# Kernel optimization log

Measured on AMD Instinct MI355X. Metric: run time of the kernel, lower is better.

## Reference

```python
import jax, jax.numpy as jnp
import numpy as np

N_HEAD = 16
QMIN, QMAX = 0.0, 255.0  # 8-bit asymmetric


def fake_quantize(x, scale, zp):
    # LearnableFakeQuantize (asymmetric, 8-bit) with straight-through round.
    q = x / scale + zp
    q = q + jax.lax.stop_gradient(jnp.round(q) - q)  # STE round
    q = jnp.clip(q, QMIN, QMAX)
    return (q - zp) * scale


def setup_inputs() -> dict:
    key = jax.random.key(0)
    ks = jax.random.split(key, 4)
    B, T, C = 2, 2048, 1024
    return {
        "hidden_states": jax.random.normal(ks[0], (B, T, C), jnp.float32),
        "W_attn": jax.random.normal(ks[1], (C, 3 * C), jnp.float32) * (1.0 / np.sqrt(C)),
        "b_attn": jnp.zeros((3 * C,), jnp.float32),
        "W_proj": jax.random.normal(ks[2], (C, C), jnp.float32) * (1.0 / np.sqrt(C)),
        "b_proj": jnp.zeros((C,), jnp.float32),
        "kv_scale": jnp.full((1,), 0.05, jnp.float32),
        "kv_zp": jnp.full((1,), 128.0, jnp.float32),
    }


def reference(hidden_states, W_attn, b_attn, W_proj, b_proj, kv_scale, kv_zp):
    B, T, C = hidden_states.shape
    H = N_HEAD
    D = C // H
    qkv = hidden_states @ W_attn + b_attn            # [B,T,3C]
    q, k, v = jnp.split(qkv, 3, axis=2)
    # [B,T,C] -> [B,H,T,D]
    q = q.reshape(B, T, H, D).transpose(0, 2, 1, 3)
    k = k.reshape(B, T, H, D).transpose(0, 2, 1, 3)
    v = v.reshape(B, T, H, D).transpose(0, 2, 1, 3)
    k = fake_quantize(k, kv_scale, kv_zp)
    v = fake_quantize(v, kv_scale, kv_zp)
    scores = jnp.einsum("bhqd,bhkd->bhqk", q, k) / jnp.sqrt(jnp.asarray(D, q.dtype))
    causal = jnp.tril(jnp.ones((T, T), bool))        # bias[:T,:T]
    scores = jnp.where(causal, scores, jnp.asarray(-jnp.inf, scores.dtype))
    attn = jax.nn.softmax(scores, axis=-1)
    out = jnp.einsum("bhqk,bhkd->bhqd", attn, v)     # [B,H,T,D]
    out = out.transpose(0, 2, 1, 3).reshape(B, T, C)
    return out @ W_proj + b_proj
```

## Files before the change

### kernel.cpp

```cpp
#include <hip/hip_runtime.h>
#include <math.h>

#define TB 2048
#define CC 1024
#define NH 16
#define HD 64

typedef __bf16 bf16x8 __attribute__((ext_vector_type(8)));
typedef __bf16 bf16x4 __attribute__((ext_vector_type(4)));
typedef float  f32x4  __attribute__((ext_vector_type(4)));

__device__ inline float exp2fast(float x) { return __builtin_amdgcn_exp2f(x); }

__device__ __forceinline__ void gl_lds16(const __bf16* g, __bf16* l) {
    __builtin_amdgcn_global_load_lds(
        (const __attribute__((address_space(1))) void*)g,
        (__attribute__((address_space(3))) void*)l, 16, 0, 0);
}

__global__ __launch_bounds__(256)
void prep_kernel(const float* __restrict__ hidden, __bf16* __restrict__ hb,
                 const float* __restrict__ Wa, __bf16* __restrict__ wat,
                 const float* __restrict__ Wp, __bf16* __restrict__ wpt)
{
    __shared__ __bf16 L[64][68];
    const int tid = threadIdx.x;
    const int bid = blockIdx.x;
    if (bid < 4096) {
        int i = (bid * 256 + tid) * 4;
        f32x4 v = *(const f32x4*)&hidden[i];
        bf16x4 o;
        o.x = (__bf16)v.x; o.y = (__bf16)v.y; o.z = (__bf16)v.z; o.w = (__bf16)v.w;
        *(bf16x4*)&hb[i] = o;
        return;
    }
    const float* src; __bf16* dst; int N, n0, k0;
    if (bid < 4096 + 768) {
        int t = bid - 4096;
        src = Wa; dst = wat; N = 3072;
        n0 = (t % 48) * 64; k0 = (t / 48) * 64;
    } else {
        int t = bid - 4864;
        src = Wp; dst = wpt; N = 1024;
        n0 = (t % 16) * 64; k0 = (t / 16) * 64;
    }
    #pragma unroll
    for (int i = 0; i < 4; i++) {
        int id = tid + i * 256;
        int r = id >> 4, c = (id & 15) * 4;
        f32x4 v = *(const f32x4*)&src[(size_t)(k0 + r) * N + n0 + c];
        bf16x4 o;
        o.x = (__bf16)v.x; o.y = (__bf16)v.y; o.z = (__bf16)v.z; o.w = (__bf16)v.w;
        *(bf16x4*)&L[r][c] = o;
    }
    __syncthreads();
    #pragma unroll
    for (int i = 0; i < 4; i++) {
        int id = tid + i * 256;
        int nr = id >> 4, kc = (id & 15) * 4;
        bf16x4 o;
        o.x = L[kc + 0][nr]; o.y = L[kc + 1][nr];
        o.z = L[kc + 2][nr]; o.w = L[kc + 3][nr];
        *(bf16x4*)&dst[(size_t)(n0 + nr) * 1024 + k0 + kc] = o;
    }
}

template<int BN, int MODE>
__global__ __launch_bounds__(256)
void gemm_bt(const __bf16* __restrict__ A, const __bf16* __restrict__ Bt,
             const float* __restrict__ bias,
             __bf16* __restrict__ o0, __bf16* __restrict__ o1,
             __bf16* __restrict__ o2, float* __restrict__ of,
             int M, int N, int K,
             const float* __restrict__ scp, const float* __restrict__ zpp)
{
    constexpr int NT = BN / 32;
    __shared__ __bf16 Asm[128][64];
    __shared__ __bf16 Bsm[BN][64];

    const int tid  = threadIdx.x;
    const int m0   = blockIdx.y * 128;
    const int n0   = blockIdx.x * BN;
    const int w    = tid >> 6, lane = tid & 63;
    const int wm   = (w & 1) * 64, wn = (w >> 1) * (BN / 2);
    const int r16  = lane & 15, quad = lane >> 4;
    const int srow = lane >> 3;
    const int scol = ((lane & 7) ^ srow) * 8;
    const int rsw  = r16 & 7;

    f32x4 acc[NT][4];
    #pragma unroll
    for (int i = 0; i < NT; i++)
        #pragma unroll
        for (int j = 0; j < 4; j++) acc[i][j] = 0.f;

    for (int k0 = 0; k0 < K; k0 += 64) {
        #pragma unroll
        for (int p = 0; p < 4; p++)
            gl_lds16(&A[(size_t)(m0 + w * 32 + p * 8 + srow) * K + k0 + scol],
                     &Asm[w * 32 + p * 8][0]);
        #pragma unroll
        for (int p = 0; p < BN / 32; p++)
            gl_lds16(&Bt[(size_t)(n0 + w * (BN / 4) + p * 8 + srow) * K + k0 + scol],
                     &Bsm[w * (BN / 4) + p * 8][0]);
        __syncthreads();

        #pragma unroll
        for (int ks = 0; ks < 2; ks++) {
            const int col = ((ks * 4 + quad) ^ rsw) * 8;
            bf16x8 af[4], bfr[NT];
            #pragma unroll
            for (int mt = 0; mt < 4; mt++)
                af[mt] = *(const bf16x8*)&Asm[wm + mt * 16 + r16][col];
            #pragma unroll
            for (int nt = 0; nt < NT; nt++)
                bfr[nt] = *(const bf16x8*)&Bsm[wn + nt * 16 + r16][col];
            #pragma unroll
            for (int nt = 0; nt < NT; nt++)
                #pragma unroll
                for (int mt = 0; mt < 4; mt++)
                    acc[nt][mt] = __builtin_amdgcn_mfma_f32_16x16x32_bf16(
                        bfr[nt], af[mt], acc[nt][mt], 0, 0, 0);
        }
        __syncthreads();
    }

    const float sc = scp[0];
    const float zp = zpp[0];

    #pragma unroll
    for (int nt = 0; nt < NT; nt++) {
        #pragma unroll
        for (int mt = 0; mt < 4; mt++) {
            int gm = m0 + wm + mt * 16 + r16;
            int gn = n0 + wn + nt * 16 + quad * 4;
            f32x4 val = acc[nt][mt] + *(const f32x4*)&bias[gn];
            if (MODE == 1) {
                *(f32x4*)&of[(size_t)gm * N + gn] = val;
            } else {
                int part = gn >> 10;
                int idx  = gn & 1023;
                int h = idx >> 6, d = idx & 63;
                int b = gm >> 11, t = gm & 2047;
                size_t off = (((size_t)(b * NH + h)) * TB + t) * HD + d;
                bf16x4 st;
                if (part == 0) {
                    #pragma unroll
                    for (int r = 0; r < 4; r++)
                        st[r] = (__bf16)(val[r] * 0.18033688f);
                    *(bf16x4*)&o0[off] = st;
                } else {
                    #pragma unroll
                    for (int r = 0; r < 4; r++) {
                        float qv = val[r] / sc + zp;
                        qv = rintf(qv);
                        qv = fminf(fmaxf(qv, 0.f), 255.f);
                        st[r] = (__bf16)((qv - zp) * sc);
                    }
                    if (part == 1) *(bf16x4*)&o1[off] = st;
                    else           *(bf16x4*)&o2[off] = st;
                }
            }
        }
    }
}

__global__ __launch_bounds__(256, 4)
void attn_mfma(const __bf16* __restrict__ Q, const __bf16* __restrict__ Kg,
               const __bf16* __restrict__ Vg, __bf16* __restrict__ O)
{
    __shared__ alignas(16) __bf16 Ksm[64][72];
    __shared__ alignas(16) __bf16 Vsm[64][72];

    const int tid  = threadIdx.x;
    const int qt   = 31 - (blockIdx.x >> 5);
    const int bh   = blockIdx.x & 31;
    const int q0   = qt * 64;
    const int w    = tid >> 6, lane = tid & 63;
    const int l15  = lane & 15, quad = lane >> 4;
    const int b    = bh >> 4, h = bh & 15;

    const int krow = tid >> 3;
    const int kseg = (tid & 7) * 8;
    const int vkey = tid & 63;
    const int vc   = tid >> 6;

    const __bf16* Kbh = Kg + (size_t)bh * TB * HD;
    const __bf16* Vbh = Vg + (size_t)bh * TB * HD;

    const __bf16* Qrow = Q + ((size_t)bh * TB + q0 + w * 16 + l15) * HD;
    bf16x8 qf0 = *(const bf16x8*)&Qrow[quad * 8];
    bf16x8 qf1 = *(const bf16x8*)&Qrow[32 + quad * 8];

    const int rbase = (l15 >> 2) * 8 + (l15 & 3);

    bf16x8 af_l;
    {
        __bf16 v = (l15 == 0) ? (__bf16)1.0f : (__bf16)0.0f;
        #pragma unroll
        for (int j = 0; j < 8; j++) af_l[j] = v;
    }

    f32x4 acc_o[4], acc_l;
    #pragma unroll
    for (int nt = 0; nt < 4; nt++) acc_o[nt] = 0.f;
    acc_l = 0.f;
    float mrun = -3.0e38f;

    bf16x8 kpre0 = *(const bf16x8*)&Kbh[(size_t)krow * HD + kseg];
    bf16x8 kpre1 = *(const bf16x8*)&Kbh[(size_t)(32 + krow) * HD + kseg];
    bf16x8 vpre0 = *(const bf16x8*)&Vbh[(size_t)vkey * HD + vc * 8];
    bf16x8 vpre1 = *(const bf16x8*)&Vbh[(size_t)vkey * HD + (4 + vc) * 8];

    for (int kt = 0; kt <= qt; kt++) {
        __syncthreads();
        *(bf16x8*)&Ksm[krow][kseg]      = kpre0;
        *(bf16x8*)&Ksm[32 + krow][kseg] = kpre1;
        #pragma unroll
        for (int j = 0; j < 8; j++) {
            Vsm[vc * 8 + j][vkey]      = vpre0[j];
            Vsm[32 + vc * 8 + j][vkey] = vpre1[j];
        }
        __syncthreads();

        if (kt < qt) {
            const __bf16* Kn = Kbh + (size_t)(kt + 1) * 64 * HD;
            const __bf16* Vn = Vbh + (size_t)(kt + 1) * 64 * HD;
            kpre0 = *(const bf16x8*)&Kn[(size_t)krow * HD + kseg];
            kpre1 = *(const bf16x8*)&Kn[(size_t)(32 + krow) * HD + kseg];
            vpre0 = *(const bf16x8*)&Vn[(size_t)vkey * HD + vc * 8];
            vpre1 = *(const bf16x8*)&Vn[(size_t)vkey * HD + (4 + vc) * 8];
        }

        const bool diag = (kt == qt);

        f32x4 s[4];
        #pragma unroll
        for (int nt = 0; nt < 4; nt++) s[nt] = 0.f;
        #pragma unroll
        for (int nt = 0; nt < 4; nt++) {
            if (diag && (nt & 1) && w < 2) continue;
            int row = rbase + (nt & 1) * 32 + ((nt >> 1) << 2);
            bf16x8 kf0 = *(const bf16x8*)&Ksm[row][quad * 8];
            bf16x8 kf1 = *(const bf16x8*)&Ksm[row][32 + quad * 8];
            s[nt] = __builtin_amdgcn_mfma_f32_16x16x32_bf16(kf0, qf0, s[nt], 0, 0, 0);
            s[nt] = __builtin_amdgcn_mfma_f32_16x16x32_bf16(kf1, qf1, s[nt], 0, 0, 0);
        }

        if (diag) {
            #pragma unroll
            for (int nt = 0; nt < 4; nt++) {
                int koff = (nt & 1) * 32 + ((nt >> 1) << 2) + quad * 8;
                #pragma unroll
                for (int r = 0; r < 4; r++)
                    if (koff + r > w * 16 + l15) s[nt][r] = -3.0e38f;
            }
        }

        float mx = s[0][0];
        #pragma unroll
        for (int nt = 0; nt < 4; nt++)
            #pragma unroll
            for (int r = 0; r < 4; r++) mx = fmaxf(mx, s[nt][r]);
        mx = fmaxf(mx, __shfl_xor(mx, 16));
        mx = fmaxf(mx, __shfl_xor(mx, 32));

        float mnew  = fmaxf(mrun, mx);
        float alpha = exp2fast(mrun - mnew);
        mrun = mnew;
        #pragma unroll
        for (int nt = 0; nt < 4; nt++)
            #pragma unroll
            for (int r = 0; r < 4; r++) acc_o[nt][r] *= alpha;
        acc_l[0] *= alpha;

        float p[4][4];
        #pragma unroll
        for (int nt = 0; nt < 4; nt++)
            #pragma unroll
            for (int r = 0; r < 4; r++) p[nt][r] = exp2fast(s[nt][r] - mnew);

        bf16x8 pf0, pf1;
        #pragma unroll
        for (int j = 0; j < 4; j++) {
            pf0[j]     = (__bf16)p[0][j];
            pf0[4 + j] = (__bf16)p[2][j];
            pf1[j]     = (__bf16)p[1][j];
            pf1[4 + j] = (__bf16)p[3][j];
        }

        acc_l = __builtin_amdgcn_mfma_f32_16x16x32_bf16(af_l, pf0, acc_l, 0, 0, 0);
        acc_l = __builtin_amdgcn_mfma_f32_16x16x32_bf16(af_l, pf1, acc_l, 0, 0, 0);

        #pragma unroll
        for (int nt = 0; nt < 4; nt++) {
            bf16x8 vf0 = *(const bf16x8*)&Vsm[nt * 16 + l15][quad * 8];
            bf16x8 vf1 = *(const bf16x8*)&Vsm[nt * 16 + l15][32 + quad * 8];
            acc_o[nt] = __builtin_amdgcn_mfma_f32_16x16x32_bf16(vf0, pf0, acc_o[nt], 0, 0, 0);
            acc_o[nt] = __builtin_amdgcn_mfma_f32_16x16x32_bf16(vf1, pf1, acc_o[nt], 0, 0, 0);
        }
    }

    float lall = __shfl(acc_l[0], l15);
    float inv  = 1.f / lall;
    size_t trow = (size_t)(b * TB) + q0 + w * 16 + l15;
    #pragma unroll
    for (int nt = 0; nt < 4; nt++) {
        bf16x4 st;
        #pragma unroll
        for (int r = 0; r < 4; r++) st[r] = (__bf16)(acc_o[nt][r] * inv);
        *(bf16x4*)&O[trow * CC + h * HD + nt * 16 + quad * 4] = st;
    }
}

extern "C" void kernel_launch(void* const* d_in, const int* in_sizes, int n_in,
                              void* d_out, int out_size, void* d_ws, size_t ws_size,
                              hipStream_t stream) {
    (void)in_sizes; (void)n_in; (void)out_size; (void)ws_size;
    const float* hidden   = (const float*)d_in[0];
    const float* W_attn   = (const float*)d_in[1];
    const float* b_attn   = (const float*)d_in[2];
    const float* W_proj   = (const float*)d_in[3];
    const float* b_proj   = (const float*)d_in[4];
    const float* kv_scale = (const float*)d_in[5];
    const float* kv_zp    = (const float*)d_in[6];
    float* out = (float*)d_out;

    __bf16* hb  = (__bf16*)d_ws;
    __bf16* wat = hb  + (size_t)4096 * 1024;
    __bf16* wpt = wat + (size_t)3072 * 1024;
    __bf16* qws = wpt + (size_t)1024 * 1024;
    __bf16* kws = qws + (size_t)2 * NH * TB * HD;
    __bf16* vws = kws + (size_t)2 * NH * TB * HD;
    __bf16* ows = vws + (size_t)2 * NH * TB * HD;

    prep_kernel<<<5120, 256, 0, stream>>>(hidden, hb, W_attn, wat, W_proj, wpt);

    gemm_bt<128, 0><<<dim3(24, 32), 256, 0, stream>>>(
        hb, wat, b_attn, qws, kws, vws, nullptr, 4096, 3072, 1024, kv_scale, kv_zp);

    attn_mfma<<<dim3(32 * 32), 256, 0, stream>>>(qws, kws, vws, ows);

    gemm_bt<64, 1><<<dim3(16, 32), 256, 0, stream>>>(
        ows, wpt, b_proj, nullptr, nullptr, nullptr, out, 4096, 1024, 1024,
        kv_scale, kv_zp);
}
```

Baseline: 182.3 us.

## Use 128-row query tiles in attention and store V transposed from QKV GEMM

The attention kernel now processes 128 query rows per block, with each wave handling two 16-row chunks, so every K/V tile loaded into shared memory serves twice as many queries. Blocks are ordered to interleave heavy and light causal tiles. The QKV GEMM epilogue writes V in a transposed [d][t] layout, which lets attention stage V with vector shared-memory stores instead of scalar transposing writes. K rows are permuted on store so fragment reads become contiguous. In exchange, the transposed V epilogue uses scattered 2-byte global stores, register use per thread grows, and only half as many blocks are launched.

```diff
diff --git a/kernel.cpp b/kernel.cpp
--- a/kernel.cpp
+++ b/kernel.cpp
@@ -142,9 +142,9 @@
                 int idx  = gn & 1023;
                 int h = idx >> 6, d = idx & 63;
                 int b = gm >> 11, t = gm & 2047;
-                size_t off = (((size_t)(b * NH + h)) * TB + t) * HD + d;
                 bf16x4 st;
                 if (part == 0) {
+                    size_t off = (((size_t)(b * NH + h)) * TB + t) * HD + d;
                     #pragma unroll
                     for (int r = 0; r < 4; r++)
                         st[r] = (__bf16)(val[r] * 0.18033688f);
@@ -157,42 +157,53 @@
                         qv = fminf(fmaxf(qv, 0.f), 255.f);
                         st[r] = (__bf16)((qv - zp) * sc);
                     }
-                    if (part == 1) *(bf16x4*)&o1[off] = st;
-                    else           *(bf16x4*)&o2[off] = st;
+                    if (part == 1) {
+                        size_t off = (((size_t)(b * NH + h)) * TB + t) * HD + d;
+                        *(bf16x4*)&o1[off] = st;
+                    } else {
+                        size_t offv = (((size_t)(b * NH + h)) * HD + d) * TB + t;
+                        #pragma unroll
+                        for (int r = 0; r < 4; r++)
+                            o2[offv + (size_t)r * TB] = st[r];
+                    }
                 }
             }
         }
     }
 }
 
-__global__ __launch_bounds__(256, 4)
+__global__ __launch_bounds__(256)
 void attn_mfma(const __bf16* __restrict__ Q, const __bf16* __restrict__ Kg,
-               const __bf16* __restrict__ Vg, __bf16* __restrict__ O)
+               const __bf16* __restrict__ Vt, __bf16* __restrict__ O)
 {
     __shared__ alignas(16) __bf16 Ksm[64][72];
     __shared__ alignas(16) __bf16 Vsm[64][72];
 
-    const int tid  = threadIdx.x;
-    const int qt   = 31 - (blockIdx.x >> 5);
-    const int bh   = blockIdx.x & 31;
-    const int q0   = qt * 64;
-    const int w    = tid >> 6, lane = tid & 63;
-    const int l15  = lane & 15, quad = lane >> 4;
-    const int b    = bh >> 4, h = bh & 15;
-
-    const int krow = tid >> 3;
-    const int kseg = (tid & 7) * 8;
-    const int vkey = tid & 63;
-    const int vc   = tid >> 6;
+    const int tid = threadIdx.x;
+    const int bid = blockIdx.x;
+    const int qb  = (bid < 256) ? 15 - (bid >> 5) : ((bid - 256) >> 5);
+    const int bh  = bid & 31;
+    const int q0  = qb * 128;
+    const int ktmax = 2 * qb + 1;
+    const int w   = tid >> 6, lane = tid & 63;
+    const int l15 = lane & 15, quad = lane >> 4;
+    const int b   = bh >> 4, h = bh & 15;
+
+    const int srow = tid >> 3;
+    const int sseg = (tid & 7) * 8;
+    const int p0 = ((srow >> 2) & 1) * 32 + ((srow >> 3) & 3) * 4 + (srow & 3);
+    const int p1 = p0 + 16;
 
     const __bf16* Kbh = Kg + (size_t)bh * TB * HD;
-    const __bf16* Vbh = Vg + (size_t)bh * TB * HD;
-
-    const __bf16* Qrow = Q + ((size_t)bh * TB + q0 + w * 16 + l15) * HD;
-    bf16x8 qf0 = *(const bf16x8*)&Qrow[quad * 8];
-    bf16x8 qf1 = *(const bf16x8*)&Qrow[32 + quad * 8];
-
-    const int rbase = (l15 >> 2) * 8 + (l15 & 3);
+    const __bf16* Vbh = Vt + (size_t)bh * HD * TB;
+
+    bf16x8 qf[2][2];
+    #pragma unroll
+    for (int c = 0; c < 2; c++) {
+        const __bf16* Qrow = Q + ((size_t)bh * TB + q0 + w * 32 + c * 16 + l15) * HD;
+        qf[c][0] = *(const bf16x8*)&Qrow[quad * 8];
+        qf[c][1] = *(const bf16x8*)&Qrow[32 + quad * 8];
+    }
 
     bf16x8 af_l;
     {
@@ -201,115 +212,141 @@
         for (int j = 0; j < 8; j++) af_l[j] = v;
     }
 
-    f32x4 acc_o[4], acc_l;
-    #pragma unroll
-    for (int nt = 0; nt < 4; nt++) acc_o[nt] = 0.f;
-    acc_l = 0.f;
-    float mrun = -3.0e38f;
-
-    bf16x8 kpre0 = *(const bf16x8*)&Kbh[(size_t)krow * HD + kseg];
-    bf16x8 kpre1 = *(const bf16x8*)&Kbh[(size_t)(32 + krow) * HD + kseg];
-    bf16x8 vpre0 = *(const bf16x8*)&Vbh[(size_t)vkey * HD + vc * 8];
-    bf16x8 vpre1 = *(const bf16x8*)&Vbh[(size_t)vkey * HD + (4 + vc) * 8];
-
-    for (int kt = 0; kt <= qt; kt++) {
+    f32x4 acc_o[2][4], acc_l[2];
+    #pragma unroll
+    for (int c = 0; c < 2; c++) {
+        #pragma unroll
+        for (int nt = 0; nt < 4; nt++) acc_o[c][nt] = 0.f;
+        acc_l[c] = 0.f;
+    }
+    float mrun[2] = {-3.0e38f, -3.0e38f};
+
+    bf16x8 kpre0 = *(const bf16x8*)&Kbh[(size_t)srow * HD + sseg];
+    bf16x8 kpre1 = *(const bf16x8*)&Kbh[(size_t)(32 + srow) * HD + sseg];
+    bf16x8 vpre0 = *(const bf16x8*)&Vbh[(size_t)srow * TB + sseg];
+    bf16x8 vpre1 = *(const bf16x8*)&Vbh[(size_t)(32 + srow) * TB + sseg];
+
+    for (int kt = 0; kt <= ktmax; kt++) {
         __syncthreads();
-        *(bf16x8*)&Ksm[krow][kseg]      = kpre0;
-        *(bf16x8*)&Ksm[32 + krow][kseg] = kpre1;
-        #pragma unroll
-        for (int j = 0; j < 8; j++) {
-            Vsm[vc * 8 + j][vkey]      = vpre0[j];
-            Vsm[32 + vc * 8 + j][vkey] = vpre1[j];
-        }
+        *(bf16x8*)&Ksm[p0][sseg]        = kpre0;
+        *(bf16x8*)&Ksm[p1][sseg]        = kpre1;
+        *(bf16x8*)&Vsm[srow][sseg]      = vpre0;
+        *(bf16x8*)&Vsm[32 + srow][sseg] = vpre1;
         __syncthreads();
 
-        if (kt < qt) {
+        if (kt < ktmax) {
             const __bf16* Kn = Kbh + (size_t)(kt + 1) * 64 * HD;
-            const __bf16* Vn = Vbh + (size_t)(kt + 1) * 64 * HD;
-            kpre0 = *(const bf16x8*)&Kn[(size_t)krow * HD + kseg];
-            kpre1 = *(const bf16x8*)&Kn[(size_t)(32 + krow) * HD + kseg];
-            vpre0 = *(const bf16x8*)&Vn[(size_t)vkey * HD + vc * 8];
-            vpre1 = *(const bf16x8*)&Vn[(size_t)vkey * HD + (4 + vc) * 8];
-        }
-
-        const bool diag = (kt == qt);
-
-        f32x4 s[4];
-        #pragma unroll
-        for (int nt = 0; nt < 4; nt++) s[nt] = 0.f;
+            kpre0 = *(const bf16x8*)&Kn[(size_t)srow * HD + sseg];
+            kpre1 = *(const bf16x8*)&Kn[(size_t)(32 + srow) * HD + sseg];
+            const int cb = (kt + 1) * 64;
+            vpre0 = *(const bf16x8*)&Vbh[(size_t)srow * TB + cb + sseg];
+            vpre1 = *(const bf16x8*)&Vbh[(size_t)(32 + srow) * TB + cb + sseg];
+        }
+
+        const int kbase = kt * 64;
+        const int qmax0 = q0 + w * 32 + 15;
+        const int qmax1 = qmax0 + 16;
+        const bool act0 = (kbase <= qmax0);
+        const bool act1 = (kbase <= qmax1);
+
+        f32x4 s[2][4];
+        #pragma unroll
+        for (int c = 0; c < 2; c++)
+            #pragma unroll
+            for (int nt = 0; nt < 4; nt++) s[c][nt] = 0.f;
         #pragma unroll
         for (int nt = 0; nt < 4; nt++) {
-            if (diag && (nt & 1) && w < 2) continue;
-            int row = rbase + (nt & 1) * 32 + ((nt >> 1) << 2);
-            bf16x8 kf0 = *(const bf16x8*)&Ksm[row][quad * 8];
-            bf16x8 kf1 = *(const bf16x8*)&Ksm[row][32 + quad * 8];
-            s[nt] = __builtin_amdgcn_mfma_f32_16x16x32_bf16(kf0, qf0, s[nt], 0, 0, 0);
-            s[nt] = __builtin_amdgcn_mfma_f32_16x16x32_bf16(kf1, qf1, s[nt], 0, 0, 0);
-        }
-
-        if (diag) {
-            #pragma unroll
-            for (int nt = 0; nt < 4; nt++) {
-                int koff = (nt & 1) * 32 + ((nt >> 1) << 2) + quad * 8;
-                #pragma unroll
-                for (int r = 0; r < 4; r++)
-                    if (koff + r > w * 16 + l15) s[nt][r] = -3.0e38f;
-            }
-        }
-
-        float mx = s[0][0];
-        #pragma unroll
-        for (int nt = 0; nt < 4; nt++)
-            #pragma unroll
-            for (int r = 0; r < 4; r++) mx = fmaxf(mx, s[nt][r]);
-        mx = fmaxf(mx, __shfl_xor(mx, 16));
-        mx = fmaxf(mx, __shfl_xor(mx, 32));
-
-        float mnew  = fmaxf(mrun, mx);
-        float alpha = exp2fast(mrun - mnew);
-        mrun = mnew;
-        #pragma unroll
-        for (int nt = 0; nt < 4; nt++)
-            #pragma unroll
-            for (int r = 0; r < 4; r++) acc_o[nt][r] *= alpha;
-        acc_l[0] *= alpha;
-
-        float p[4][4];
-        #pragma unroll
-        for (int nt = 0; nt < 4; nt++)
-            #pragma unroll
-            for (int r = 0; r < 4; r++) p[nt][r] = exp2fast(s[nt][r] - mnew);
-
-        bf16x8 pf0, pf1;
-        #pragma unroll
-        for (int j = 0; j < 4; j++) {
-            pf0[j]     = (__bf16)p[0][j];
-            pf0[4 + j] = (__bf16)p[2][j];
-            pf1[j]     = (__bf16)p[1][j];
-            pf1[4 + j] = (__bf16)p[3][j];
-        }
-
-        acc_l = __builtin_amdgcn_mfma_f32_16x16x32_bf16(af_l, pf0, acc_l, 0, 0, 0);
-        acc_l = __builtin_amdgcn_mfma_f32_16x16x32_bf16(af_l, pf1, acc_l, 0, 0, 0);
+            const int kmin = kbase + (nt & 1) * 32 + ((nt >> 1) << 2);
+            if (kmin > qmax1) continue;
+            bf16x8 kf0 = *(const bf16x8*)&Ksm[nt * 16 + l15][quad * 8];
+            bf16x8 kf1 = *(const bf16x8*)&Ksm[nt * 16 + l15][32 + quad * 8];
+            if (act0 && kmin <= qmax0) {
+                s[0][nt] = __builtin_amdgcn_mfma_f32_16x16x32_bf16(kf0, qf[0][0], s[0][nt], 0, 0, 0);
+                s[0][nt] = __builtin_amdgcn_mfma_f32_16x16x32_bf16(kf1, qf[0][1], s[0][nt], 0, 0, 0);
+            }
+            if (act1) {
+                s[1][nt] = __builtin_amdgcn_mfma_f32_16x16x32_bf16(kf0, qf[1][0], s[1][nt], 0, 0, 0);
+                s[1][nt] = __builtin_amdgcn_mfma_f32_16x16x32_bf16(kf1, qf[1][1], s[1][nt], 0, 0, 0);
+            }
+        }
+
+        bf16x8 pf[2][2];
+        #pragma unroll
+        for (int c = 0; c < 2; c++) {
+            const bool act = c ? act1 : act0;
+            if (!act) continue;
+            const int qlo = q0 + w * 32 + c * 16;
+            if (kbase + 63 > qlo) {
+                const int qg = qlo + l15;
+                #pragma unroll
+                for (int nt = 0; nt < 4; nt++) {
+                    const int koff = kbase + (nt & 1) * 32 + ((nt >> 1) << 2) + quad * 8;
+                    #pragma unroll
+                    for (int r = 0; r < 4; r++)
+                        if (koff + r > qg) s[c][nt][r] = -3.0e38f;
+                }
+            }
+            float mx = s[c][0][0];
+            #pragma unroll
+            for (int nt = 0; nt < 4; nt++)
+                #pragma unroll
+                for (int r = 0; r < 4; r++) mx = fmaxf(mx, s[c][nt][r]);
+            mx = fmaxf(mx, __shfl_xor(mx, 16));
+            mx = fmaxf(mx, __shfl_xor(mx, 32));
+
+            float mnew  = fmaxf(mrun[c], mx);
+            float alpha = exp2fast(mrun[c] - mnew);
+            mrun[c] = mnew;
+            #pragma unroll
+            for (int nt = 0; nt < 4; nt++)
+                #pragma unroll
+                for (int r = 0; r < 4; r++) acc_o[c][nt][r] *= alpha;
+            acc_l[c][0] *= alpha;
+
+            float p[4][4];
+            #pragma unroll
+            for (int nt = 0; nt < 4; nt++)
+                #pragma unroll
+                for (int r = 0; r < 4; r++) p[nt][r] = exp2fast(s[c][nt][r] - mnew);
+
+            #pragma unroll
+            for (int j = 0; j < 4; j++) {
+                pf[c][0][j]     = (__bf16)p[0][j];
+                pf[c][0][4 + j] = (__bf16)p[2][j];
+                pf[c][1][j]     = (__bf16)p[1][j];
+                pf[c][1][4 + j] = (__bf16)p[3][j];
+            }
+            acc_l[c] = __builtin_amdgcn_mfma_f32_16x16x32_bf16(af_l, pf[c][0], acc_l[c], 0, 0, 0);
+            acc_l[c] = __builtin_amdgcn_mfma_f32_16x16x32_bf16(af_l, pf[c][1], acc_l[c], 0, 0, 0);
+        }
 
         #pragma unroll
         for (int nt = 0; nt < 4; nt++) {
             bf16x8 vf0 = *(const bf16x8*)&Vsm[nt * 16 + l15][quad * 8];
             bf16x8 vf1 = *(const bf16x8*)&Vsm[nt * 16 + l15][32 + quad * 8];
-            acc_o[nt] = __builtin_amdgcn_mfma_f32_16x16x32_bf16(vf0, pf0, acc_o[nt], 0, 0, 0);
-            acc_o[nt] = __builtin_amdgcn_mfma_f32_16x16x32_bf16(vf1, pf1, acc_o[nt], 0, 0, 0);
-        }
-    }
-
-    float lall = __shfl(acc_l[0], l15);
-    float inv  = 1.f / lall;
-    size_t trow = (size_t)(b * TB) + q0 + w * 16 + l15;
-    #pragma unroll
-    for (int nt = 0; nt < 4; nt++) {
-        bf16x4 st;
-        #pragma unroll
-        for (int r = 0; r < 4; r++) st[r] = (__bf16)(acc_o[nt][r] * inv);
-        *(bf16x4*)&O[trow * CC + h * HD + nt * 16 + quad * 4] = st;
+            if (act0) {
+                acc_o[0][nt] = __builtin_amdgcn_mfma_f32_16x16x32_bf16(vf0, pf[0][0], acc_o[0][nt], 0, 0, 0);
+                acc_o[0][nt] = __builtin_amdgcn_mfma_f32_16x16x32_bf16(vf1, pf[0][1], acc_o[0][nt], 0, 0, 0);
+            }
+            if (act1) {
+                acc_o[1][nt] = __builtin_amdgcn_mfma_f32_16x16x32_bf16(vf0, pf[1][0], acc_o[1][nt], 0, 0, 0);
+                acc_o[1][nt] = __builtin_amdgcn_mfma_f32_16x16x32_bf16(vf1, pf[1][1], acc_o[1][nt], 0, 0, 0);
+            }
+        }
+    }
+
+    #pragma unroll
+    for (int c = 0; c < 2; c++) {
+        float lall = __shfl(acc_l[c][0], l15);
+        float inv  = 1.f / lall;
+        size_t trow = (size_t)(b * TB) + q0 + w * 32 + c * 16 + l15;
+        #pragma unroll
+        for (int nt = 0; nt < 4; nt++) {
+            bf16x4 st;
+            #pragma unroll
+            for (int r = 0; r < 4; r++) st[r] = (__bf16)(acc_o[c][nt][r] * inv);
+            *(bf16x4*)&O[trow * CC + h * HD + nt * 16 + quad * 4] = st;
+        }
     }
 }
 
@@ -339,7 +376,7 @@
     gemm_bt<128, 0><<<dim3(24, 32), 256, 0, stream>>>(
         hb, wat, b_attn, qws, kws, vws, nullptr, 4096, 3072, 1024, kv_scale, kv_zp);
 
-    attn_mfma<<<dim3(32 * 32), 256, 0, stream>>>(qws, kws, vws, ows);
+    attn_mfma<<<dim3(512), 256, 0, stream>>>(qws, kws, vws, ows);
 
     gemm_bt<64, 1><<<dim3(16, 32), 256, 0, stream>>>(
         ows, wpt, b_proj, nullptr, nullptr, nullptr, out, 4096, 1024, 1024,
```

Measured after the change: 201.8 us. 1.11x slower.

## Store V transposed from QKV GEMM and stage K/V to LDS with vector writes

Applied to the files above, without the earlier changes.

The QKV GEMM epilogue now writes V in a [b,h,d,t] transposed layout, so the attention kernel can load V tiles as contiguous 16-byte rows and store them to LDS with vector writes. Before, it did eight scalar transposing LDS stores per thread. K rows are permuted into LDS on the store side, so fragment reads become simple row indexing. The causal mask check is generalized to absolute indices. The GEMM epilogue now issues strided scalar 2-byte stores for V, which may cost more global write bandwidth. The attention kernel's launch-bounds occupancy hint is also dropped.

```diff
diff --git a/kernel.cpp b/kernel.cpp
--- a/kernel.cpp
+++ b/kernel.cpp
@@ -142,9 +142,9 @@
                 int idx  = gn & 1023;
                 int h = idx >> 6, d = idx & 63;
                 int b = gm >> 11, t = gm & 2047;
-                size_t off = (((size_t)(b * NH + h)) * TB + t) * HD + d;
                 bf16x4 st;
                 if (part == 0) {
+                    size_t off = (((size_t)(b * NH + h)) * TB + t) * HD + d;
                     #pragma unroll
                     for (int r = 0; r < 4; r++)
                         st[r] = (__bf16)(val[r] * 0.18033688f);
@@ -157,43 +157,48 @@
                         qv = fminf(fmaxf(qv, 0.f), 255.f);
                         st[r] = (__bf16)((qv - zp) * sc);
                     }
-                    if (part == 1) *(bf16x4*)&o1[off] = st;
-                    else           *(bf16x4*)&o2[off] = st;
+                    if (part == 1) {
+                        size_t off = (((size_t)(b * NH + h)) * TB + t) * HD + d;
+                        *(bf16x4*)&o1[off] = st;
+                    } else {
+                        size_t offv = (((size_t)(b * NH + h)) * HD + d) * TB + t;
+                        #pragma unroll
+                        for (int r = 0; r < 4; r++)
+                            o2[offv + (size_t)r * TB] = st[r];
+                    }
                 }
             }
         }
     }
 }
 
-__global__ __launch_bounds__(256, 4)
+__global__ __launch_bounds__(256)
 void attn_mfma(const __bf16* __restrict__ Q, const __bf16* __restrict__ Kg,
-               const __bf16* __restrict__ Vg, __bf16* __restrict__ O)
+               const __bf16* __restrict__ Vt, __bf16* __restrict__ O)
 {
     __shared__ alignas(16) __bf16 Ksm[64][72];
     __shared__ alignas(16) __bf16 Vsm[64][72];
 
-    const int tid  = threadIdx.x;
-    const int qt   = 31 - (blockIdx.x >> 5);
-    const int bh   = blockIdx.x & 31;
-    const int q0   = qt * 64;
-    const int w    = tid >> 6, lane = tid & 63;
-    const int l15  = lane & 15, quad = lane >> 4;
-    const int b    = bh >> 4, h = bh & 15;
-
-    const int krow = tid >> 3;
-    const int kseg = (tid & 7) * 8;
-    const int vkey = tid & 63;
-    const int vc   = tid >> 6;
+    const int tid = threadIdx.x;
+    const int qt  = 31 - (blockIdx.x >> 5);
+    const int bh  = blockIdx.x & 31;
+    const int q0  = qt * 64;
+    const int w   = tid >> 6, lane = tid & 63;
+    const int l15 = lane & 15, quad = lane >> 4;
+    const int b   = bh >> 4, h = bh & 15;
+
+    const int srow = tid >> 3;
+    const int sseg = (tid & 7) * 8;
+    const int p0 = ((srow >> 2) & 1) * 32 + ((srow >> 3) & 3) * 4 + (srow & 3);
+    const int p1 = p0 + 16;
 
     const __bf16* Kbh = Kg + (size_t)bh * TB * HD;
-    const __bf16* Vbh = Vg + (size_t)bh * TB * HD;
+    const __bf16* Vbh = Vt + (size_t)bh * HD * TB;
 
     const __bf16* Qrow = Q + ((size_t)bh * TB + q0 + w * 16 + l15) * HD;
     bf16x8 qf0 = *(const bf16x8*)&Qrow[quad * 8];
     bf16x8 qf1 = *(const bf16x8*)&Qrow[32 + quad * 8];
 
-    const int rbase = (l15 >> 2) * 8 + (l15 & 3);
-
     bf16x8 af_l;
     {
         __bf16 v = (l15 == 0) ? (__bf16)1.0f : (__bf16)0.0f;
@@ -207,53 +212,53 @@
     acc_l = 0.f;
     float mrun = -3.0e38f;
 
-    bf16x8 kpre0 = *(const bf16x8*)&Kbh[(size_t)krow * HD + kseg];
-    bf16x8 kpre1 = *(const bf16x8*)&Kbh[(size_t)(32 + krow) * HD + kseg];
-    bf16x8 vpre0 = *(const bf16x8*)&Vbh[(size_t)vkey * HD + vc * 8];
-    bf16x8 vpre1 = *(const bf16x8*)&Vbh[(size_t)vkey * HD + (4 + vc) * 8];
+    bf16x8 kpre0 = *(const bf16x8*)&Kbh[(size_t)srow * HD + sseg];
+    bf16x8 kpre1 = *(const bf16x8*)&Kbh[(size_t)(32 + srow) * HD + sseg];
+    bf16x8 vpre0 = *(const bf16x8*)&Vbh[(size_t)srow * TB + sseg];
+    bf16x8 vpre1 = *(const bf16x8*)&Vbh[(size_t)(32 + srow) * TB + sseg];
 
     for (int kt = 0; kt <= qt; kt++) {
         __syncthreads();
-        *(bf16x8*)&Ksm[krow][kseg]      = kpre0;
-        *(bf16x8*)&Ksm[32 + krow][kseg] = kpre1;
-        #pragma unroll
-        for (int j = 0; j < 8; j++) {
-            Vsm[vc * 8 + j][vkey]      = vpre0[j];
-            Vsm[32 + vc * 8 + j][vkey] = vpre1[j];
-        }
+        *(bf16x8*)&Ksm[p0][sseg]        = kpre0;
+        *(bf16x8*)&Ksm[p1][sseg]        = kpre1;
+        *(bf16x8*)&Vsm[srow][sseg]      = vpre0;
+        *(bf16x8*)&Vsm[32 + srow][sseg] = vpre1;
         __syncthreads();
 
         if (kt < qt) {
             const __bf16* Kn = Kbh + (size_t)(kt + 1) * 64 * HD;
-            const __bf16* Vn = Vbh + (size_t)(kt + 1) * 64 * HD;
-            kpre0 = *(const bf16x8*)&Kn[(size_t)krow * HD + kseg];
-            kpre1 = *(const bf16x8*)&Kn[(size_t)(32 + krow) * HD + kseg];
-            vpre0 = *(const bf16x8*)&Vn[(size_t)vkey * HD + vc * 8];
-            vpre1 = *(const bf16x8*)&Vn[(size_t)vkey * HD + (4 + vc) * 8];
-        }
-
-        const bool diag = (kt == qt);
+            kpre0 = *(const bf16x8*)&Kn[(size_t)srow * HD + sseg];
+            kpre1 = *(const bf16x8*)&Kn[(size_t)(32 + srow) * HD + sseg];
+            const int cb = (kt + 1) * 64;
+            vpre0 = *(const bf16x8*)&Vbh[(size_t)srow * TB + cb + sseg];
+            vpre1 = *(const bf16x8*)&Vbh[(size_t)(32 + srow) * TB + cb + sseg];
+        }
+
+        const int kbase = kt * 64;
+        const int qlo   = q0 + w * 16;
+        const int qmax  = qlo + 15;
 
         f32x4 s[4];
         #pragma unroll
         for (int nt = 0; nt < 4; nt++) s[nt] = 0.f;
         #pragma unroll
         for (int nt = 0; nt < 4; nt++) {
-            if (diag && (nt & 1) && w < 2) continue;
-            int row = rbase + (nt & 1) * 32 + ((nt >> 1) << 2);
-            bf16x8 kf0 = *(const bf16x8*)&Ksm[row][quad * 8];
-            bf16x8 kf1 = *(const bf16x8*)&Ksm[row][32 + quad * 8];
+            const int kmin = kbase + (nt & 1) * 32 + ((nt >> 1) << 2);
+            if (kmin > qmax) continue;
+            bf16x8 kf0 = *(const bf16x8*)&Ksm[nt * 16 + l15][quad * 8];
+            bf16x8 kf1 = *(const bf16x8*)&Ksm[nt * 16 + l15][32 + quad * 8];
             s[nt] = __builtin_amdgcn_mfma_f32_16x16x32_bf16(kf0, qf0, s[nt], 0, 0, 0);
             s[nt] = __builtin_amdgcn_mfma_f32_16x16x32_bf16(kf1, qf1, s[nt], 0, 0, 0);
         }
 
-        if (diag) {
+        if (kbase + 63 > qlo) {
+            const int qg = qlo + l15;
             #pragma unroll
             for (int nt = 0; nt < 4; nt++) {
-                int koff = (nt & 1) * 32 + ((nt >> 1) << 2) + quad * 8;
+                const int koff = kbase + (nt & 1) * 32 + ((nt >> 1) << 2) + quad * 8;
                 #pragma unroll
                 for (int r = 0; r < 4; r++)
-                    if (koff + r > w * 16 + l15) s[nt][r] = -3.0e38f;
+                    if (koff + r > qg) s[nt][r] = -3.0e38f;
             }
         }
 
@@ -339,7 +344,7 @@
     gemm_bt<128, 0><<<dim3(24, 32), 256, 0, stream>>>(
         hb, wat, b_attn, qws, kws, vws, nullptr, 4096, 3072, 1024, kv_scale, kv_zp);
 
-    attn_mfma<<<dim3(32 * 32), 256, 0, stream>>>(qws, kws, vws, ows);
+    attn_mfma<<<dim3(1024), 256, 0, stream>>>(qws, kws, vws, ows);
 
     gemm_bt<64, 1><<<dim3(16, 32), 256, 0, stream>>>(
         ows, wpt, b_proj, nullptr, nullptr, nullptr, out, 4096, 1024, 1024,
```

New measurement: 184.3 us. About the same (+1.1%).
